# Optimization experiments

Measured on AMD Instinct MI355X. Metric: run time of the kernel, lower is better.

## Reference

```python
import jax, jax.numpy as jnp
import numpy as np

# ---- dopri5 (RK45) tableau ----
C2, C3, C4, C5 = 1/5, 3/10, 4/5, 8/9
A21 = 1/5
A31, A32 = 3/40, 9/40
A41, A42, A43 = 44/45, -56/15, 32/9
A51, A52, A53, A54 = 19372/6561, -25360/2187, 64448/6561, -212/729
A61, A62, A63, A64, A65 = 9017/3168, -355/33, 46732/5247, 49/176, -5103/18656
B1, B3, B4, B5, B6 = 35/384, 500/1113, 125/192, -2187/6784, 11/84
# error coefficients = b(5th) - b(4th)
E1, E3, E4, E5, E6, E7 = 71/57600, -71/16695, 71/1920, -17253/339200, 22/525, -1/40

N_STEPS = 24          # fixed scan length for the adaptive loop (jit-friendly)
RTOL = ATOL = 1e-3    # tolerance from init_kwargs
DT0 = 0.1             # initial step size


def conv_time(t, x, w, b, padding):
    # append time as an extra channel, then NCHW conv
    t_img = jnp.full_like(x[:, :1], t)
    xt = jnp.concatenate([t_img, x], axis=1)
    y = jax.lax.conv_general_dilated(xt, w, (1, 1), padding,
                                     dimension_numbers=('NCHW', 'OIHW', 'NCHW'))
    return y + b[None, :, None, None]


def ode_func(t, x, w1, b1, w2, b2, w3, b3):
    h = jax.nn.relu(conv_time(t, x, w1, b1, [(0, 0), (0, 0)]))
    h = jax.nn.relu(conv_time(t, h, w2, b2, [(1, 1), (1, 1)]))
    return conv_time(t, h, w3, b3, [(0, 0), (0, 0)])


def dopri5_step(f, t, y, dt):
    k1 = f(t, y)
    k2 = f(t + dt * C2, y + dt * (A21 * k1))
    k3 = f(t + dt * C3, y + dt * (A31 * k1 + A32 * k2))
    k4 = f(t + dt * C4, y + dt * (A41 * k1 + A42 * k2 + A43 * k3))
    k5 = f(t + dt * C5, y + dt * (A51 * k1 + A52 * k2 + A53 * k3 + A54 * k4))
    k6 = f(t + dt, y + dt * (A61 * k1 + A62 * k2 + A63 * k3 + A64 * k4 + A65 * k5))
    y5 = y + dt * (B1 * k1 + B3 * k3 + B4 * k4 + B5 * k5 + B6 * k6)
    k7 = f(t + dt, y5)  # FSAL stage, used for error estimate
    err = dt * (E1 * k1 + E3 * k3 + E4 * k4 + E5 * k5 + E6 * k6 + E7 * k7)
    return y5, err


def integrate(f, y0):
    """Adaptive dopri5 from t=0 to t=1 with fixed-length masked scan."""
    def step(carry, _):
        t, y, dt = carry
        dt_c = jnp.minimum(dt, 1.0 - t)
        y_new, err = dopri5_step(f, t, y, dt_c)
        tol = ATOL + RTOL * jnp.maximum(jnp.abs(y), jnp.abs(y_new))
        err_norm = jnp.sqrt(jnp.mean((err / tol) ** 2))
        done = t >= 1.0 - 1e-7
        adv = (err_norm <= 1.0) & (~done)
        t_n = jnp.where(adv, t + dt_c, t)
        y_n = jnp.where(adv, y_new, y)
        safe = jnp.maximum(err_norm, 1e-10)
        factor = jnp.clip(0.9 * safe ** (-0.2), 0.2, 10.0)
        dt_n = jnp.where(done, dt, dt_c * factor)
        return (t_n, y_n, dt_n), None

    step = jax.checkpoint(step)
    (t, y, dt), _ = jax.lax.scan(step,
                                 (jnp.float32(0.0), y0, jnp.float32(DT0)),
                                 None, length=N_STEPS)
    return y


def setup_inputs() -> dict:
    key = jax.random.key(0)
    ks = jax.random.split(key, 9)
    B, Cin, H, W = 64, 3, 32, 32
    AUG, NF = 5, 64
    CH = Cin + AUG  # 8
    x = jax.random.normal(ks[0], (B, Cin, H, W), dtype=jnp.float32)
    def wgt(k, shape):
        fan_in = shape[1] * shape[2] * shape[3]
        return jax.random.normal(k, shape, dtype=jnp.float32) / np.sqrt(fan_in).astype(np.float32)
    w1 = wgt(ks[1], (NF, CH + 1, 1, 1)); b1 = jnp.zeros((NF,), jnp.float32)
    w2 = wgt(ks[2], (NF, NF + 1, 3, 3)); b2 = jnp.zeros((NF,), jnp.float32)
    w3 = wgt(ks[3], (CH, NF + 1, 1, 1)); b3 = jnp.zeros((CH,), jnp.float32)
    flat = CH * H * W  # 8192
    wl = jax.random.normal(ks[4], (10, flat), dtype=jnp.float32) / np.sqrt(flat).astype(np.float32)
    bl = jnp.zeros((10,), jnp.float32)
    return {"x": x, "w1": w1, "b1": b1, "w2": w2, "b2": b2,
            "w3": w3, "b3": b3, "wl": wl, "bl": bl}


def reference(x, w1, b1, w2, b2, w3, b3, wl, bl):
    B, C, H, W = x.shape
    AUG = w3.shape[0] - C  # augmented channels
    aug = jnp.zeros((B, AUG, H, W), dtype=x.dtype)
    y0 = jnp.concatenate([x, aug], axis=1)
    f = lambda t, y: ode_func(t, y, w1, b1, w2, b2, w3, b3)
    yT = integrate(f, y0)                    # state at t = 1
    out = yT.reshape(B, -1) @ wl.T + bl      # final linear head
    return out
```

## Files before the change

kernel.cpp:

```cpp
#include <hip/hip_runtime.h>
#include <math.h>

namespace {
constexpr int BN = 64;
constexpr int HW = 1024;
constexpr int NS = BN*8*HW;

constexpr float C2f = 0.2f, C3f = 0.3f, C4f = 0.8f, C5f = (float)(8.0/9.0);
constexpr float A21 = 0.2f;
constexpr float A31 = (float)(3.0/40.0),  A32 = (float)(9.0/40.0);
constexpr float A41 = (float)(44.0/45.0), A42 = (float)(-56.0/15.0), A43 = (float)(32.0/9.0);
constexpr float A51 = (float)(19372.0/6561.0), A52 = (float)(-25360.0/2187.0),
                A53 = (float)(64448.0/6561.0), A54 = (float)(-212.0/729.0);
constexpr float A61 = (float)(9017.0/3168.0), A62 = (float)(-355.0/33.0),
                A63 = (float)(46732.0/5247.0), A64 = (float)(49.0/176.0),
                A65 = (float)(-5103.0/18656.0);
constexpr float B1c = (float)(35.0/384.0), B3c = (float)(500.0/1113.0),
                B4c = (float)(125.0/192.0), B5c = (float)(-2187.0/6784.0),
                B6c = (float)(11.0/84.0);
constexpr float E1c = (float)(71.0/57600.0), E3c = (float)(-71.0/16695.0),
                E4c = (float)(71.0/1920.0), E5c = (float)(-17253.0/339200.0),
                E6c = (float)(22.0/525.0),  E7c = (float)(-1.0/40.0);
constexpr float RTOL = 1e-3f, ATOL = 1e-3f;

constexpr size_t OFF_PART = 0;
constexpr size_t OFF_FLAG = 1024;
constexpr size_t OFF_CNT  = 1536;
constexpr size_t OFF_TSUM = 1600;
constexpr size_t OFF_W2P  = 2176;
constexpr size_t OFF_Y    = 20608;
constexpr size_t OFF_Y5   = OFF_Y  + (size_t)NS;
constexpr size_t OFF_K    = OFF_Y5 + (size_t)NS;
constexpr size_t OFF_WPK  = OFF_K + (size_t)7*NS;
constexpr size_t OFF_FT   = OFF_WPK + 1152;
constexpr size_t OFF_FB   = OFF_FT + 512;

constexpr int ACT_STRIDE = 272;
constexpr int H2_STRIDE  = 144;
}

__constant__ float g_cf[6][5] = {
    {A21, 0, 0, 0, 0},
    {A31, A32, 0, 0, 0},
    {A41, A42, A43, 0, 0},
    {A51, A52, A53, A54, 0},
    {A61, A62, A63, A64, A65},
    {0, 0, 0, 0, 0}};
__constant__ float g_ct[6] = {C2f, C3f, C4f, C5f, 1.0f, 1.0f};

typedef _Float16 hfrag8 __attribute__((ext_vector_type(8)));
typedef float f32x16 __attribute__((ext_vector_type(16)));

union HU { hfrag8 h; unsigned u[4]; uint4 v; };

__device__ __forceinline__ float ld_sysf(const float* p) {
    return __hip_atomic_load(p, __ATOMIC_RELAXED, __HIP_MEMORY_SCOPE_SYSTEM);
}
__device__ __forceinline__ float2 ld_sysf2(const float* p) {
    union { unsigned long long u; float2 f; } c;
    c.u = __hip_atomic_load((const unsigned long long*)p, __ATOMIC_RELAXED,
                            __HIP_MEMORY_SCOPE_SYSTEM);
    return c.f;
}
__device__ __forceinline__ void st_sysf(float* p, float v) {
    __hip_atomic_store(p, v, __ATOMIC_RELAXED, __HIP_MEMORY_SCOPE_SYSTEM);
}
__device__ __forceinline__ void st_sysf2(float* p, float a, float b) {
    union { unsigned long long u; float2 f; } c;
    c.f = make_float2(a, b);
    __hip_atomic_store((unsigned long long*)p, c.u, __ATOMIC_RELAXED,
                       __HIP_MEMORY_SCOPE_SYSTEM);
}

__device__ __forceinline__ void ld8(const float* p, float* v, bool sys) {
    if (sys) {
        #pragma unroll
        for (int h = 0; h < 4; h++) {
            float2 t = ld_sysf2(p + 2*h);
            v[2*h] = t.x; v[2*h+1] = t.y;
        }
    } else {
        float4 a = *(const float4*)p;
        float4 b = *(const float4*)(p + 4);
        v[0]=a.x; v[1]=a.y; v[2]=a.z; v[3]=a.w;
        v[4]=b.x; v[5]=b.y; v[6]=b.z; v[7]=b.w;
    }
}
__device__ __forceinline__ void st8(float* p, const float* v, bool sys) {
    if (sys) {
        st_sysf2(p,     v[0], v[1]);
        st_sysf2(p + 2, v[2], v[3]);
        st_sysf2(p + 4, v[4], v[5]);
        st_sysf2(p + 6, v[6], v[7]);
    } else {
        *(float4*)p       = make_float4(v[0], v[1], v[2], v[3]);
        *(float4*)(p + 4) = make_float4(v[4], v[5], v[6], v[7]);
    }
}

__global__ __launch_bounds__(256)
void k_init(const float* __restrict__ x, float* __restrict__ y,
            int* __restrict__ flags, int* __restrict__ flagT,
            int* __restrict__ flagB)
{
    int idx = blockIdx.x*256 + threadIdx.x;
    int b = idx >> 13, px = (idx >> 3) & 1023, c = idx & 7;
    y[idx] = (c < 3) ? x[(size_t)(b*3 + c)*1024 + px] : 0.0f;
    if (idx < 512) { flags[idx] = 0; flagT[idx] = 0; flagB[idx] = 0; }
}

__global__ __launch_bounds__(256)
void k_prepack(const float* __restrict__ w1, const float* __restrict__ w2,
               const float* __restrict__ w3, _Float16* __restrict__ w2p,
               float* __restrict__ tsum, float* __restrict__ wpk)
{
    int gid = blockIdx.x*256 + threadIdx.x;
    if (gid < 36864) {
        int j    = gid & 7;
        int lane = (gid >> 3) & 63;
        int nt   = (gid >> 9) & 1;
        int ks   = (gid >> 10) & 3;
        int tap  = gid >> 12;
        int oc = nt*32 + (lane & 31);
        int kpos = ks*16 + (lane >> 5)*8 + j;
        int oct = kpos >> 5, q2b = (kpos >> 4) & 1, rr = kpos & 15;
        int ic = oct*32 + (rr & 3) + (q2b << 2) + ((rr >> 2) << 3);
        w2p[gid] = (_Float16)w2[oc*585 + (1 + ic)*9 + tap];
    }
    if (gid < 576) {
        int oc = gid & 63, combo = gid >> 6;
        int rcase = combo / 3, ccase = combo % 3;
        float s = 0.0f;
        for (int kh = 0; kh < 3; kh++) {
            if ((rcase == 1 && kh == 0) || (rcase == 2 && kh == 2)) continue;
            for (int kw = 0; kw < 3; kw++) {
                if ((ccase == 1 && kw == 0) || (ccase == 2 && kw == 2)) continue;
                s += w2[oc*585 + kh*3 + kw];
            }
        }
        tsum[gid] = s;
    }
    if (gid < 512) wpk[gid] = w1[(gid & 63)*9 + 1 + (gid >> 6)];
    if (gid < 64)  wpk[512 + gid] = w1[gid*9];
    if (gid < 512) wpk[576 + gid] = w3[(gid & 7)*65 + 1 + (gid >> 3)];
    if (gid < 8)   wpk[1088 + gid] = w3[gid*65];
}

__global__ void __launch_bounds__(256, 2)
k_ode(const float* __restrict__ b1, const float* __restrict__ b2,
      const float* __restrict__ b3, const _Float16* __restrict__ w2p,
      const float* __restrict__ tsumg, const float* __restrict__ wpk,
      const float* __restrict__ wl, const float* __restrict__ bl,
      float* __restrict__ ybuf, float* __restrict__ y5buf,
      float* __restrict__ kb, float* __restrict__ part,
      int* __restrict__ flags, int* __restrict__ flagT,
      int* __restrict__ flagB, float* __restrict__ out)
{
    __shared__ __align__(16) unsigned char s_pool[192*ACT_STRIDE];
    __shared__ __align__(16) unsigned char s_h2[128*H2_STRIDE];
    __shared__ float s_tsum[576];
    __shared__ float s_b2v[64], s_b1v[64], s_w10v[64];
    __shared__ float s_w30v[8], s_b3v[8];
    __shared__ float s_red[8];

    const int tid = threadIdx.x;
    const int nblk = gridDim.x;
    const int lane = tid & 63;
    const int m32 = lane & 31, q2 = lane >> 5;
    const int rp = tid >> 7;
    const int np = (tid >> 6) & 1;
    const int wid = tid >> 6;
    const bool lz32 = (lane == 32);
    const bool lz31 = (lane == 31);

    if (tid < 64) {
        s_b2v[tid] = b2[tid];
        s_b1v[tid] = b1[tid];
        s_w10v[tid] = wpk[512 + tid];
    }
    if (tid < 8) { s_w30v[tid] = wpk[1088 + tid]; s_b3v[tid] = b3[tid]; }
    for (int i = tid; i < 576; i += 256) s_tsum[i] = tsumg[i];
    __syncthreads();

    hfrag8 w1lo[2], w1hi[2];
    #pragma unroll
    for (int oct = 0; oct < 2; oct++)
        #pragma unroll
        for (int j = 0; j < 8; j++) {
            _Float16 wv = (_Float16)wpk[j*64 + oct*32 + m32];
            w1lo[oct][j] = q2 ? (_Float16)0.0f : wv;
            w1hi[oct][j] = q2 ? wv : (_Float16)0.0f;
        }
    hfrag8 w3f[4];
    #pragma unroll
    for (int kst = 0; kst < 4; kst++)
        #pragma unroll
        for (int j = 0; j < 8; j++) {
            int kpos = kst*16 + q2*8 + j;
            int oct = kpos >> 5, q2b = (kpos >> 4) & 1, rr = kpos & 15;
            int ch = oct*32 + (rr & 3) + (q2b << 2) + ((rr >> 2) << 3);
            w3f[kst][j] = (m32 < 8) ? (_Float16)wpk[576 + ch*8 + m32]
                                    : (_Float16)0.0f;
        }

    float t = 0.0f, dt = 0.1f;
    float* ya = ybuf; float* yb = y5buf;
    float* ka = kb;  float* kg = kb + 6*(size_t)NS;

    auto wait_all = [&](int target) {
        for (;;) {
            bool ok = (__hip_atomic_load(&flags[tid], __ATOMIC_RELAXED,
                           __HIP_MEMORY_SCOPE_SYSTEM) >= target)
                   && (__hip_atomic_load(&flags[tid + 256], __ATOMIC_RELAXED,
                           __HIP_MEMORY_SCOPE_SYSTEM) >= target);
            if (__syncthreads_and((int)ok)) break;
            __builtin_amdgcn_s_sleep(2);
        }
    };

    auto eval = [&](const float* src, int nc, const float* cf, float ctv,
                    float* kout, int mode, int gev, float* partp) {
        float dtc = fminf(dt, 1.0f - t);
        float ts  = t + ctv*dtc;

        for (int tile = blockIdx.x; tile < 512; tile += nblk) {
            int b = tile >> 3, rg = tile & 7;

            auto zload = [&](int lr) {
                HU pz; pz.v = make_uint4(0u,0u,0u,0u);
                int r = rg*4 - 1 + lr;
                if ((unsigned)lr < 6u && (unsigned)r < 32u) {
                    bool nbr = (lr == 0) | (lr == 5);
                    int px = (r << 5) + m32;
                    size_t pb8 = ((size_t)(b << 10) + px) << 3;
                    float kv[5][8], sv[8];
                    if (nbr) {
                        #pragma unroll
                        for (int j = 0; j < 5; j++) if (j < nc) {
                            const float* kp = (j == 0 ? ka : kb + (size_t)j*NS) + pb8;
                            #pragma unroll
                            for (int h = 0; h < 4; h++) {
                                float2 t2 = ld_sysf2(kp + 2*h);
                                kv[j][2*h] = t2.x; kv[j][2*h+1] = t2.y;
                            }
                        }
                        #pragma unroll
                        for (int h = 0; h < 4; h++) {
                            float2 t2 = ld_sysf2(src + pb8 + 2*h);
                            sv[2*h] = t2.x; sv[2*h+1] = t2.y;
                        }
                    } else {
                        #pragma unroll
                        for (int j = 0; j < 5; j++) if (j < nc) {
                            const float* kp = (j == 0 ? ka : kb + (size_t)j*NS) + pb8;
                            float4 a4 = *(const float4*)kp;
                            float4 b4 = *(const float4*)(kp + 4);
                            kv[j][0]=a4.x; kv[j][1]=a4.y; kv[j][2]=a4.z; kv[j][3]=a4.w;
                            kv[j][4]=b4.x; kv[j][5]=b4.y; kv[j][6]=b4.z; kv[j][7]=b4.w;
                        }
                        float4 a4 = *(const float4*)(src + pb8);
                        float4 b4 = *(const float4*)(src + pb8 + 4);
                        sv[0]=a4.x; sv[1]=a4.y; sv[2]=a4.z; sv[3]=a4.w;
                        sv[4]=b4.x; sv[5]=b4.y; sv[6]=b4.z; sv[7]=b4.w;
                    }
                    float s[8] = {0,0,0,0,0,0,0,0};
                    #pragma unroll
                    for (int j = 0; j < 5; j++) if (j < nc) {
                        float a = cf[j];
                        #pragma unroll
                        for (int c = 0; c < 8; c++) s[c] = fmaf(a, kv[j][c], s[c]);
                    }
                    #pragma unroll
                    for (int c = 0; c < 8; c++)
                        pz.h[c] = (_Float16)(sv[c] + dtc*s[c]);
                }
                return pz;
            };

            HU pz;
            if (q2 == 0) pz = zload(wid + 1);
            if (gev > 1 && q2 == 1 && (wid == 0 || wid == 3)) {
                bool need = (wid == 0) ? (rg > 0) : (rg < 7);
                if (need) {
                    const int* fp = (wid == 0) ? &flagB[tile-1] : &flagT[tile+1];
                    while (__hip_atomic_load(fp, __ATOMIC_RELAXED,
                                             __HIP_MEMORY_SCOPE_SYSTEM) < gev-1)
                        __builtin_amdgcn_s_sleep(1);
                }
            }
            if (q2 == 1) pz = zload((wid == 0) ? 0 : ((wid == 3) ? 5 : -1));

            auto wr_act = [&](int lr, const f32x16& a1, int oct, bool valid) {
                unsigned words[8];
                #pragma unroll
                for (int pr = 0; pr < 8; pr++) {
                    int r0 = 2*pr;
                    int oc0 = oct*32 + (r0 & 3) + 8*(r0 >> 2) + 4*q2;
                    float v0 = valid ? fmaxf(a1[r0]   + ts*s_w10v[oc0]
                                             + s_b1v[oc0],   0.0f) : 0.0f;
                    float v1 = valid ? fmaxf(a1[r0+1] + ts*s_w10v[oc0+1]
                                             + s_b1v[oc0+1], 0.0f) : 0.0f;
                    union { _Float16 h[2]; unsigned u; } pk;
                    pk.h[0] = (_Float16)v0; pk.h[1] = (_Float16)v1;
                    words[pr] = pk.u;
                }
                unsigned char* basep = s_pool + (size_t)(lr*32 + m32)*ACT_STRIDE
                                       + oct*64 + q2*32;
                *(uint4*)basep        = make_uint4(words[0],words[1],words[2],words[3]);
                *(uint4*)(basep + 16) = make_uint4(words[4],words[5],words[6],words[7]);
            };
            {
                f32x16 zz = (f32x16)(0.0f);
                f32x16 c0 = __builtin_amdgcn_mfma_f32_32x32x16_f16(w1lo[0], pz.h, zz, 0,0,0);
                f32x16 c1 = __builtin_amdgcn_mfma_f32_32x32x16_f16(w1lo[1], pz.h, zz, 0,0,0);
                wr_act(wid + 1, c0, 0, true);
                wr_act(wid + 1, c1, 1, true);
                if (wid == 0 || wid == 3) {
                    int lrh = (wid == 0) ? 0 : 5;
                    bool vh = (unsigned)(rg*4 - 1 + lrh) < 32u;
                    f32x16 d0 = __builtin_amdgcn_mfma_f32_32x32x16_f16(w1hi[0], pz.h, zz, 0,0,0);
                    f32x16 d1 = __builtin_amdgcn_mfma_f32_32x32x16_f16(w1hi[1], pz.h, zz, 0,0,0);
                    wr_act(lrh, d0, 0, vh);
                    wr_act(lrh, d1, 1, vh);
                }
            }
            __syncthreads();

            f32x16 acc2[2];
            acc2[0] = (f32x16)(0.0f);
            acc2[1] = (f32x16)(0.0f);
            {
                const unsigned char* actb = (const unsigned char*)s_pool;
                #pragma unroll 1
                for (int ks = 0; ks < 4; ks++) {
                    HU fc[4], d0[4], d2[4];
                    #pragma unroll
                    for (int l = 0; l < 4; l++) {
                        const unsigned char* p = actb
                            + (size_t)((rp*2 + l)*32 + m32)*ACT_STRIDE
                            + ks*32 + q2*16;
                        fc[l].v = *(const uint4*)p;
                    }
                    #pragma unroll
                    for (int l = 0; l < 4; l++) {
                        #pragma unroll
                        for (int i = 0; i < 4; i++) {
                            unsigned s0 = (unsigned)__builtin_amdgcn_update_dpp(
                                0, (int)fc[l].u[i], 0x138, 0xF, 0xF, true);
                            d0[l].u[i] = lz32 ? 0u : s0;
                            unsigned s2 = (unsigned)__builtin_amdgcn_update_dpp(
                                0, (int)fc[l].u[i], 0x130, 0xF, 0xF, true);
                            d2[l].u[i] = lz31 ? 0u : s2;
                        }
                    }
                    #pragma unroll
                    for (int kh = 0; kh < 3; kh++) {
                        #pragma unroll
                        for (int kw = 0; kw < 3; kw++) {
                            int tap = kh*3 + kw;
                            hfrag8 aw = *(const hfrag8*)
                                (w2p + (size_t)((tap*4 + ks)*2 + np)*512 + lane*8);
                            #pragma unroll
                            for (int ri = 0; ri < 2; ri++) {
                                int l = ri + kh;
                                hfrag8 bf = (kw == 0) ? d0[l].h
                                          : ((kw == 1) ? fc[l].h : d2[l].h);
                                acc2[ri] = __builtin_amdgcn_mfma_f32_32x32x16_f16(
                                    aw, bf, acc2[ri], 0, 0, 0);
                            }
                        }
                    }
                }
            }

            {
                int ccase = (m32 == 0) ? 1 : ((m32 == 31) ? 2 : 0);
                #pragma unroll
                for (int ri = 0; ri < 2; ri++) {
                    int pg = rp*2 + ri;
                    int r_out = rg*4 + pg;
                    int rcase = (r_out == 0) ? 1 : ((r_out == 31) ? 2 : 0);
                    const float* tsb = &s_tsum[(rcase*3 + ccase)*64];
                    int px = pg*32 + m32;
                    unsigned words[8];
                    #pragma unroll
                    for (int pr = 0; pr < 8; pr++) {
                        int r0 = 2*pr;
                        int oc0 = np*32 + (r0 & 3) + 8*(r0 >> 2) + 4*q2;
                        float v0 = fmaxf(acc2[ri][r0]   + ts*tsb[oc0]
                                         + s_b2v[oc0],   0.0f);
                        float v1 = fmaxf(acc2[ri][r0+1] + ts*tsb[oc0+1]
                                         + s_b2v[oc0+1], 0.0f);
                        union { _Float16 h[2]; unsigned u; } pk;
                        pk.h[0] = (_Float16)v0; pk.h[1] = (_Float16)v1;
                        words[pr] = pk.u;
                    }
                    unsigned char* basep = s_h2 + (size_t)px*H2_STRIDE
                                           + np*64 + q2*32;
                    *(uint4*)basep        = make_uint4(words[0],words[1],words[2],words[3]);
                    *(uint4*)(basep + 16) = make_uint4(words[4],words[5],words[6],words[7]);
                }
            }
            __syncthreads();

            float ls = 0.0f;
            {
                f32x16 a3a = (f32x16)(0.0f);
                #pragma unroll
                for (int kst = 0; kst < 4; kst++) {
                    HU f;
                    const unsigned char* p = s_h2
                        + (size_t)(wid*32 + m32)*H2_STRIDE + kst*32 + q2*16;
                    f.v = *(const uint4*)p;
                    a3a = __builtin_amdgcn_mfma_f32_32x32x16_f16(
                        w3f[kst], f.h, a3a, 0, 0, 0);
                }
                float a3[8];
                #pragma unroll
                for (int r = 0; r < 4; r++) {
                    float own = a3a[r];
                    float oth = __shfl(own, lane ^ 32, 64);
                    a3[r]     = q2 ? oth : own;
                    a3[4 + r] = q2 ? own : oth;
                }
                if (q2 == 0) {
                    #pragma unroll
                    for (int c = 0; c < 8; c++)
                        a3[c] += fmaf(ts, s_w30v[c], s_b3v[c]);
                    bool sysrow = (wid == 0) | (wid == 3);
                    int px = rg*128 + wid*32 + m32;
                    size_t pb8 = ((size_t)(b << 10) + px) << 3;
                    st8(kout + pb8, a3, sysrow);
                    if (mode == 1) {
                        float kv1[8], kv3[8], kv4[8], kv5[8], yv[8], r8[8];
                        ld8(ka + pb8, kv1, false);
                        ld8(kb + 2*(size_t)NS + pb8, kv3, false);
                        ld8(kb + 3*(size_t)NS + pb8, kv4, false);
                        ld8(kb + 4*(size_t)NS + pb8, kv5, false);
                        ld8(ya + pb8, yv, false);
                        #pragma unroll
                        for (int c = 0; c < 8; c++)
                            r8[c] = yv[c] + dtc*(B1c*kv1[c] + B3c*kv3[c]
                                    + B4c*kv4[c] + B5c*kv5[c] + B6c*a3[c]);
                        st8(yb + pb8, r8, sysrow);
                    } else if (mode == 2) {
                        float kv1[8], kv3[8], kv4[8], kv5[8], kv6[8], yv[8], y5v[8];
                        ld8(ka + pb8, kv1, false);
                        ld8(kb + 2*(size_t)NS + pb8, kv3, false);
                        ld8(kb + 3*(size_t)NS + pb8, kv4, false);
                        ld8(kb + 4*(size_t)NS + pb8, kv5, false);
                        ld8(kb + 5*(size_t)NS + pb8, kv6, false);
                        ld8(ya + pb8, yv, false);
                        ld8(yb + pb8, y5v, false);
                        #pragma unroll
                        for (int c = 0; c < 8; c++) {
                            float e = dtc*(E1c*kv1[c] + E3c*kv3[c] + E4c*kv4[c]
                                           + E5c*kv5[c] + E6c*kv6[c] + E7c*a3[c]);
                            float tol = ATOL + RTOL*fmaxf(fabsf(yv[c]), fabsf(y5v[c]));
                            float rr = e / tol;
                            ls += rr*rr;
                        }
                    }
                }
            }
            asm volatile("s_waitcnt vmcnt(0)" ::: "memory");
            if (lane == 0 && wid == 0)
                __hip_atomic_store(&flagT[tile], gev, __ATOMIC_RELAXED,
                                   __HIP_MEMORY_SCOPE_SYSTEM);
            if (lane == 0 && wid == 3)
                __hip_atomic_store(&flagB[tile], gev, __ATOMIC_RELAXED,
                                   __HIP_MEMORY_SCOPE_SYSTEM);
            if (mode == 2) {
                float v = ls;
                #pragma unroll
                for (int off = 1; off < 64; off <<= 1)
                    v += __shfl_xor(v, off, 64);
                if (lane == 0) s_red[wid] = v;
                __syncthreads();
                if (tid == 0) {
                    st_sysf(&partp[tile],
                            s_red[0] + s_red[1] + s_red[2] + s_red[3]);
                    asm volatile("s_waitcnt vmcnt(0)" ::: "memory");
                    __hip_atomic_store(&flags[tile], gev, __ATOMIC_RELAXED,
                                       __HIP_MEMORY_SCOPE_SYSTEM);
                }
            }
        }
    };

    int gev = 1;
    eval(ya, 0, g_cf[5], 0.0f, ka, 0, gev, part);
    gev++;

    for (int st = 0; st < 24; st++) {
        if (t >= 1.0f - 1e-7f) break;
        float* partp = part + (size_t)(st & 1)*512;
        for (int e = 0; e < 6; e++) {
            int nc = (e < 5) ? e + 1 : 0;
            const float* src = (e == 5) ? yb : ya;
            float* kout = (e < 5) ? kb + (size_t)(e + 1)*NS : kg;
            int mode = (e == 4) ? 1 : ((e == 5) ? 2 : 0);
            eval(src, nc, g_cf[e], g_ct[e], kout, mode, gev, partp);
            gev++;
        }
        wait_all(gev - 1);
        float v = ld_sysf(&partp[tid]) + ld_sysf(&partp[tid + 256]);
        #pragma unroll
        for (int off = 1; off < 64; off <<= 1)
            v += __shfl_xor(v, off, 64);
        if (lane == 0) s_red[wid] = v;
        __syncthreads();
        float red0 = s_red[0] + s_red[1] + s_red[2] + s_red[3];
        float err_norm = sqrtf(red0 / (float)NS);
        float dtc = fminf(dt, 1.0f - t);
        bool adv = (err_norm <= 1.0f);
        if (adv) {
            t = t + dtc;
            float* tmp = ya; ya = yb; yb = tmp;
            tmp = ka; ka = kg; kg = tmp;
        }
        float safe = fmaxf(err_norm, 1e-10f);
        float factor = fminf(fmaxf(0.9f*powf(safe, -0.2f), 0.2f), 10.0f);
        dt = dtc*factor;
    }

    for (int tile = blockIdx.x; tile < 512; tile += nblk) {
        int b = tile >> 3, rg = tile & 7;
        if (tid < 128) {
            int lrow = tid >> 5;
            if (lrow == 1 || lrow == 2) {
                int px = rg*128 + tid;
                float* yp = ya + (((size_t)(b << 10) + px) << 3);
                float4 v0 = *(const float4*)yp;
                float4 v1 = *(const float4*)(yp + 4);
                st_sysf2(yp,     v0.x, v0.y);
                st_sysf2(yp + 2, v0.z, v0.w);
                st_sysf2(yp + 4, v1.x, v1.y);
                st_sysf2(yp + 6, v1.z, v1.w);
            }
        }
    }
    __syncthreads();
    for (int tile = blockIdx.x; tile < 512; tile += nblk)
        if (tid == 0)
            __hip_atomic_store(&flags[tile], gev, __ATOMIC_RELAXED,
                               __HIP_MEMORY_SCOPE_SYSTEM);
    wait_all(gev);

    for (int bh = blockIdx.x; bh < 64; bh += nblk) {
        float* s_hred = (float*)s_pool;
        float acc[10];
        #pragma unroll
        for (int m = 0; m < 10; m++) acc[m] = 0.0f;
        for (int px = tid; px < 1024; px += 256) {
            const float* yp = ya + (((size_t)(bh << 10) + px) << 3);
            float yv[8];
            #pragma unroll
            for (int h = 0; h < 4; h++) {
                float2 v = ld_sysf2(yp + 2*h);
                yv[2*h] = v.x; yv[2*h+1] = v.y;
            }
            #pragma unroll
            for (int c = 0; c < 8; c++) {
                float v = yv[c];
                #pragma unroll
                for (int m = 0; m < 10; m++)
                    acc[m] = fmaf(v, wl[(size_t)m*8192 + (c << 10) + px], acc[m]);
            }
        }
        #pragma unroll
        for (int m = 0; m < 10; m++) s_hred[m*256 + tid] = acc[m];
        __syncthreads();
        for (int sft = 128; sft > 0; sft >>= 1) {
            if (tid < sft) {
                #pragma unroll
                for (int m = 0; m < 10; m++)
                    s_hred[m*256 + tid] += s_hred[m*256 + tid + sft];
            }
            __syncthreads();
        }
        if (tid < 10) out[bh*10 + tid] = s_hred[tid*256] + bl[tid];
        __syncthreads();
    }
}

extern "C" void kernel_launch(void* const* d_in, const int* in_sizes, int n_in,
                              void* d_out, int out_size, void* d_ws, size_t ws_size,
                              hipStream_t stream)
{
    const float* x  = (const float*)d_in[0];
    const float* w1 = (const float*)d_in[1];
    const float* b1 = (const float*)d_in[2];
    const float* w2 = (const float*)d_in[3];
    const float* b2 = (const float*)d_in[4];
    const float* w3 = (const float*)d_in[5];
    const float* b3 = (const float*)d_in[6];
    const float* wl = (const float*)d_in[7];
    const float* bl = (const float*)d_in[8];
    float* out = (float*)d_out;

    float* F = (float*)d_ws;
    float* part = F + OFF_PART;
    int*   flags = (int*)(F + OFF_FLAG);
    float* tsum = F + OFF_TSUM;
    _Float16* w2p = (_Float16*)(F + OFF_W2P);
    float* y    = F + OFF_Y;
    float* y5   = F + OFF_Y5;
    float* kbp  = F + OFF_K;
    float* wpk  = F + OFF_WPK;
    int*   flagT = (int*)(F + OFF_FT);
    int*   flagB = (int*)(F + OFF_FB);

    k_init<<<NS/256, 256, 0, stream>>>(x, y, flags, flagT, flagB);
    k_prepack<<<144, 256, 0, stream>>>(w1, w2, w3, w2p, tsum, wpk);

    int maxb = 0;
    if (hipOccupancyMaxActiveBlocksPerMultiprocessor(&maxb,
            reinterpret_cast<const void*>(k_ode), 256, 0) != hipSuccess || maxb < 1)
        maxb = 1;
    int cus = 256;
    {
        int dev = 0;
        hipGetDevice(&dev);
        hipDeviceProp_t prop;
        if (hipGetDeviceProperties(&prop, dev) == hipSuccess && prop.multiProcessorCount > 0)
            cus = prop.multiProcessorCount;
    }
    long cap = (long)maxb * (long)cus;
    int gridn = (int)((cap < 512) ? cap : 512);
    if (gridn < 16) gridn = 16;

    k_ode<<<gridn, 256, 0, stream>>>(b1, b2, b3, w2p, tsum, wpk, wl, bl,
                                     y, y5, kbp, part, flags, flagT, flagB, out);
}
```

Measured before the change: 399.3 us.

## Compute edge rows first and publish halo flags before interior rows

```diff
diff --git a/kernel.cpp b/kernel.cpp
--- a/kernel.cpp
+++ b/kernel.cpp
@@ -263,16 +263,16 @@
                         sv[0]=a4.x; sv[1]=a4.y; sv[2]=a4.z; sv[3]=a4.w;
                         sv[4]=b4.x; sv[5]=b4.y; sv[6]=b4.z; sv[7]=b4.w;
                     }
-                    float s[8] = {0,0,0,0,0,0,0,0};
+                    float s_[8] = {0,0,0,0,0,0,0,0};
                     #pragma unroll
                     for (int j = 0; j < 5; j++) if (j < nc) {
                         float a = cf[j];
                         #pragma unroll
-                        for (int c = 0; c < 8; c++) s[c] = fmaf(a, kv[j][c], s[c]);
+                        for (int c = 0; c < 8; c++) s_[c] = fmaf(a, kv[j][c], s_[c]);
                     }
                     #pragma unroll
                     for (int c = 0; c < 8; c++)
-                        pz.h[c] = (_Float16)(sv[c] + dtc*s[c]);
+                        pz.h[c] = (_Float16)(sv[c] + dtc*s_[c]);
                 }
                 return pz;
             };
@@ -326,31 +326,29 @@
             }
             __syncthreads();
 
-            f32x16 acc2[2];
-            acc2[0] = (f32x16)(0.0f);
-            acc2[1] = (f32x16)(0.0f);
-            {
-                const unsigned char* actb = (const unsigned char*)s_pool;
+            const unsigned char* actb = (const unsigned char*)s_pool;
+
+            auto conv2row = [&](int pg, f32x16& acc) {
                 #pragma unroll 1
                 for (int ks = 0; ks < 4; ks++) {
-                    HU fc[4], d0[4], d2[4];
+                    HU fc[3], d0[3], d2[3];
                     #pragma unroll
-                    for (int l = 0; l < 4; l++) {
+                    for (int i = 0; i < 3; i++) {
                         const unsigned char* p = actb
-                            + (size_t)((rp*2 + l)*32 + m32)*ACT_STRIDE
+                            + (size_t)((pg + i)*32 + m32)*ACT_STRIDE
                             + ks*32 + q2*16;
-                        fc[l].v = *(const uint4*)p;
+                        fc[i].v = *(const uint4*)p;
                     }
                     #pragma unroll
-                    for (int l = 0; l < 4; l++) {
-                        #pragma unroll
-                        for (int i = 0; i < 4; i++) {
+                    for (int i = 0; i < 3; i++) {
+                        #pragma unroll
+                        for (int u = 0; u < 4; u++) {
                             unsigned s0 = (unsigned)__builtin_amdgcn_update_dpp(
-                                0, (int)fc[l].u[i], 0x138, 0xF, 0xF, true);
-                            d0[l].u[i] = lz32 ? 0u : s0;
+                                0, (int)fc[i].u[u], 0x138, 0xF, 0xF, true);
+                            d0[i].u[u] = lz32 ? 0u : s0;
                             unsigned s2 = (unsigned)__builtin_amdgcn_update_dpp(
-                                0, (int)fc[l].u[i], 0x130, 0xF, 0xF, true);
-                            d2[l].u[i] = lz31 ? 0u : s2;
+                                0, (int)fc[i].u[u], 0x130, 0xF, 0xF, true);
+                            d2[i].u[u] = lz31 ? 0u : s2;
                         }
                     }
                     #pragma unroll
@@ -360,51 +358,40 @@
                             int tap = kh*3 + kw;
                             hfrag8 aw = *(const hfrag8*)
                                 (w2p + (size_t)((tap*4 + ks)*2 + np)*512 + lane*8);
-                            #pragma unroll
-                            for (int ri = 0; ri < 2; ri++) {
-                                int l = ri + kh;
-                                hfrag8 bf = (kw == 0) ? d0[l].h
-                                          : ((kw == 1) ? fc[l].h : d2[l].h);
-                                acc2[ri] = __builtin_amdgcn_mfma_f32_32x32x16_f16(
-                                    aw, bf, acc2[ri], 0, 0, 0);
-                            }
+                            hfrag8 bf = (kw == 0) ? d0[kh].h
+                                      : ((kw == 1) ? fc[kh].h : d2[kh].h);
+                            acc = __builtin_amdgcn_mfma_f32_32x32x16_f16(
+                                aw, bf, acc, 0, 0, 0);
                         }
                     }
                 }
-            }
-
-            {
+            };
+
+            auto h2epi = [&](int pg, const f32x16& acc) {
                 int ccase = (m32 == 0) ? 1 : ((m32 == 31) ? 2 : 0);
+                int r_out = rg*4 + pg;
+                int rcase = (r_out == 0) ? 1 : ((r_out == 31) ? 2 : 0);
+                const float* tsb = &s_tsum[(rcase*3 + ccase)*64];
+                int px = pg*32 + m32;
+                unsigned words[8];
                 #pragma unroll
-                for (int ri = 0; ri < 2; ri++) {
-                    int pg = rp*2 + ri;
-                    int r_out = rg*4 + pg;
-                    int rcase = (r_out == 0) ? 1 : ((r_out == 31) ? 2 : 0);
-                    const float* tsb = &s_tsum[(rcase*3 + ccase)*64];
-                    int px = pg*32 + m32;
-                    unsigned words[8];
-                    #pragma unroll
-                    for (int pr = 0; pr < 8; pr++) {
-                        int r0 = 2*pr;
-                        int oc0 = np*32 + (r0 & 3) + 8*(r0 >> 2) + 4*q2;
-                        float v0 = fmaxf(acc2[ri][r0]   + ts*tsb[oc0]
-                                         + s_b2v[oc0],   0.0f);
-                        float v1 = fmaxf(acc2[ri][r0+1] + ts*tsb[oc0+1]
-                                         + s_b2v[oc0+1], 0.0f);
-                        union { _Float16 h[2]; unsigned u; } pk;
-                        pk.h[0] = (_Float16)v0; pk.h[1] = (_Float16)v1;
-                        words[pr] = pk.u;
-                    }
-                    unsigned char* basep = s_h2 + (size_t)px*H2_STRIDE
-                                           + np*64 + q2*32;
-                    *(uint4*)basep        = make_uint4(words[0],words[1],words[2],words[3]);
-                    *(uint4*)(basep + 16) = make_uint4(words[4],words[5],words[6],words[7]);
-                }
-            }
-            __syncthreads();
+                for (int pr = 0; pr < 8; pr++) {
+                    int r0 = 2*pr;
+                    int oc0 = np*32 + (r0 & 3) + 8*(r0 >> 2) + 4*q2;
+                    float v0 = fmaxf(acc[r0]   + ts*tsb[oc0] + s_b2v[oc0],   0.0f);
+                    float v1 = fmaxf(acc[r0+1] + ts*tsb[oc0+1] + s_b2v[oc0+1], 0.0f);
+                    union { _Float16 h[2]; unsigned u; } pk;
+                    pk.h[0] = (_Float16)v0; pk.h[1] = (_Float16)v1;
+                    words[pr] = pk.u;
+                }
+                unsigned char* basep = s_h2 + (size_t)px*H2_STRIDE
+                                       + np*64 + q2*32;
+                *(uint4*)basep        = make_uint4(words[0],words[1],words[2],words[3]);
+                *(uint4*)(basep + 16) = make_uint4(words[4],words[5],words[6],words[7]);
+            };
 
             float ls = 0.0f;
-            {
+            auto conv3row = [&]() {
                 f32x16 a3a = (f32x16)(0.0f);
                 #pragma unroll
                 for (int kst = 0; kst < 4; kst++) {
@@ -427,10 +414,10 @@
                     #pragma unroll
                     for (int c = 0; c < 8; c++)
                         a3[c] += fmaf(ts, s_w30v[c], s_b3v[c]);
-                    bool sysrow = (wid == 0) | (wid == 3);
+                    bool edge = (wid == 0) | (wid == 3);
                     int px = rg*128 + wid*32 + m32;
                     size_t pb8 = ((size_t)(b << 10) + px) << 3;
-                    st8(kout + pb8, a3, sysrow);
+                    st8(kout + pb8, a3, edge);
                     if (mode == 1) {
                         float kv1[8], kv3[8], kv4[8], kv5[8], yv[8], r8[8];
                         ld8(ka + pb8, kv1, false);
@@ -442,7 +429,7 @@
                         for (int c = 0; c < 8; c++)
                             r8[c] = yv[c] + dtc*(B1c*kv1[c] + B3c*kv3[c]
                                     + B4c*kv4[c] + B5c*kv5[c] + B6c*a3[c]);
-                        st8(yb + pb8, r8, sysrow);
+                        st8(yb + pb8, r8, edge);
                     } else if (mode == 2) {
                         float kv1[8], kv3[8], kv4[8], kv5[8], kv6[8], yv[8], y5v[8];
                         ld8(ka + pb8, kv1, false);
@@ -462,14 +449,37 @@
                         }
                     }
                 }
-            }
-            asm volatile("s_waitcnt vmcnt(0)" ::: "memory");
-            if (lane == 0 && wid == 0)
-                __hip_atomic_store(&flagT[tile], gev, __ATOMIC_RELAXED,
-                                   __HIP_MEMORY_SCOPE_SYSTEM);
-            if (lane == 0 && wid == 3)
-                __hip_atomic_store(&flagB[tile], gev, __ATOMIC_RELAXED,
-                                   __HIP_MEMORY_SCOPE_SYSTEM);
+            };
+
+            {
+                int pgE = (rp == 0) ? 0 : 3;
+                f32x16 accE = (f32x16)(0.0f);
+                conv2row(pgE, accE);
+                h2epi(pgE, accE);
+            }
+            __syncthreads();
+
+            if (wid == 0 || wid == 3) {
+                conv3row();
+                asm volatile("s_waitcnt vmcnt(0)" ::: "memory");
+                if (lane == 0 && wid == 0)
+                    __hip_atomic_store(&flagT[tile], gev, __ATOMIC_RELAXED,
+                                       __HIP_MEMORY_SCOPE_SYSTEM);
+                if (lane == 0 && wid == 3)
+                    __hip_atomic_store(&flagB[tile], gev, __ATOMIC_RELAXED,
+                                       __HIP_MEMORY_SCOPE_SYSTEM);
+            }
+
+            {
+                int pgI = (rp == 0) ? 1 : 2;
+                f32x16 accI = (f32x16)(0.0f);
+                conv2row(pgI, accI);
+                h2epi(pgI, accI);
+            }
+            __syncthreads();
+
+            if (wid == 1 || wid == 2) conv3row();
+
             if (mode == 2) {
                 float v = ls;
                 #pragma unroll
```

After: 522.1 us. 1.31x slower.
